# Optimization experiments

Hardware: AMD Instinct MI355X
Metric: run time of the kernel (lower is better)

## Reference

```python
import jax, jax.numpy as jnp
import numpy as np

D_MODEL = 512
N_HEADS = 8
HEAD_DIM = D_MODEL // N_HEADS
SEQ = 2048
BATCH = 2
EPS = 1e-5
SCALE = 1.0 / np.sqrt(HEAD_DIM).astype(np.float32)
# (kind, window, dilation) per head, matching init_kwargs head_specs
SPECS = [("global", 0, 1), ("global", 0, 1),
         ("window", 64, 1), ("window", 128, 1), ("window", 256, 1),
         ("dilated", 64, 2), ("dilated", 64, 4), ("dilated", 64, 8)]


def build_masks(N):
    i = jnp.arange(N)
    D = jnp.abs(i[:, None] - i[None, :])
    ms = []
    for kind, w, dil in SPECS:
        if kind == "global":
            ms.append(jnp.ones((N, N), dtype=bool))
        elif kind == "window":
            ms.append(D <= w)
        else:  # dilated
            ms.append((D % dil == 0) & (D // dil <= w))
    return jnp.stack(ms)  # [H, N, N] bool


def layernorm(x, g, b):
    mu = jnp.mean(x, axis=-1, keepdims=True)
    var = jnp.mean((x - mu) ** 2, axis=-1, keepdims=True)
    return (x - mu) * jax.lax.rsqrt(var + EPS) * g + b


def setup_inputs() -> dict:
    key = jax.random.key(0)
    ks = jax.random.split(key, 7)
    w = 0.02
    return {
        "x": jax.random.normal(ks[0], (BATCH, SEQ, D_MODEL), dtype=jnp.float32),
        "Wq": jax.random.normal(ks[1], (D_MODEL, D_MODEL), dtype=jnp.float32) * w,
        "Wk": jax.random.normal(ks[2], (D_MODEL, D_MODEL), dtype=jnp.float32) * w,
        "Wv": jax.random.normal(ks[3], (D_MODEL, D_MODEL), dtype=jnp.float32) * w,
        "Wo": jax.random.normal(ks[4], (D_MODEL, D_MODEL), dtype=jnp.float32) * w,
        "T_w1": jax.random.normal(ks[5], (D_MODEL, D_MODEL), dtype=jnp.float32) * w,
        "T_b1": jnp.zeros((D_MODEL,), dtype=jnp.float32),
        "T_w2": jax.random.normal(ks[6], (1, D_MODEL), dtype=jnp.float32) * w,
        "T_b2": jnp.zeros((1,), dtype=jnp.float32),
        "ln_in_g": jnp.ones((D_MODEL,), dtype=jnp.float32),
        "ln_in_b": jnp.zeros((D_MODEL,), dtype=jnp.float32),
        "ln_out_g": jnp.ones((D_MODEL,), dtype=jnp.float32),
        "ln_out_b": jnp.zeros((D_MODEL,), dtype=jnp.float32),
    }


def reference(x, Wq, Wk, Wv, Wo, T_w1, T_b1, T_w2, T_b2,
              ln_in_g, ln_in_b, ln_out_g, ln_out_b):
    B, N, H = x.shape
    x0 = x
    xn = layernorm(x, ln_in_g, ln_in_b)
    # torch Linear: y = x @ W.T ; reshape to [B, h, N, d]
    def heads(W):
        return (xn @ W.T).reshape(B, N, N_HEADS, HEAD_DIM).transpose(0, 2, 1, 3)
    Q, K, V = heads(Wq), heads(Wk), heads(Wv)
    attn = jnp.einsum("bhqd,bhkd->bhqk", Q, K) * SCALE
    mask = build_masks(N)  # [h, N, N]
    attn = jnp.where(mask[None], attn, -jnp.inf)
    attn = jax.nn.softmax(attn, axis=-1)  # every row has diagonal unmasked
    out = jnp.einsum("bhqk,bhkd->bhqd", attn, V)
    out = out.transpose(0, 2, 1, 3).reshape(B, N, N_HEADS * HEAD_DIM)
    out = out @ Wo.T
    # tanh-gated softmax over sequence dim
    T_logits = jnp.tanh(xn @ T_w1.T + T_b1) @ T_w2.T + T_b2  # [B, N, 1]
    T = jax.nn.softmax(T_logits, axis=1)
    out = out * T
    return layernorm(out + x0, ln_out_g, ln_out_b)
```

## Files before the change

### kernel.cpp

```cpp
#include <hip/hip_runtime.h>
#include <math.h>

#define N_SEQ 2048
#define DM    512
#define NTOK  4096
#define NH    8
#define HD    64
#define NSLOT 32

typedef __attribute__((ext_vector_type(8))) short short8;
typedef __attribute__((ext_vector_type(4))) short short4_t;
typedef __attribute__((ext_vector_type(4))) float f32x4;

__device__ inline short f2bf(float x) {
    union { float f; unsigned u; } v; v.f = x;
    unsigned r = v.u + 0x7fff + ((v.u >> 16) & 1);
    return (short)(r >> 16);
}
__device__ inline float bf2f(short s) {
    union { unsigned u; float f; } v; v.u = ((unsigned)(unsigned short)s) << 16;
    return v.f;
}
__device__ inline unsigned pkbf(float a, float b) {
    return ((unsigned)(unsigned short)f2bf(b) << 16) | (unsigned)(unsigned short)f2bf(a);
}
__device__ inline float ftanh(float x) {
    float e = __expf(2.f * x);
    return 1.f - 2.f / (e + 1.f);
}

__device__ inline f32x4 mfma16(short8 a, short8 b, f32x4 c) {
    return __builtin_amdgcn_mfma_f32_16x16x32_bf16(a, b, c, 0, 0, 0);
}

__device__ __forceinline__ void async_cp16(const short* g, short* l) {
    __builtin_amdgcn_global_load_lds(
        (const __attribute__((address_space(1))) void*)g,
        (__attribute__((address_space(3))) void*)l, 16, 0, 0);
}

#define QSCALE 0.1803398875f

__global__ __launch_bounds__(256) void k_lncvt(
    const float* __restrict__ x, const float* __restrict__ g,
    const float* __restrict__ b, short* __restrict__ y, float* __restrict__ lg,
    const float* __restrict__ Wq, const float* __restrict__ Wk,
    const float* __restrict__ Wv, const float* __restrict__ Tw1,
    const float* __restrict__ Wo,
    short* __restrict__ wcat, short* __restrict__ wo) {
    int blk = blockIdx.x, t = threadIdx.x;
    if (blk < 2048) {
        int sub = t >> 7, tt = t & 127;
        int tk = blk * 2 + sub;
        if (tt == 0) lg[tk] = 0.f;
        float4 xv = ((const float4*)(x + (size_t)tk * DM))[tt];
        float s = xv.x + xv.y + xv.z + xv.w;
        float q = xv.x*xv.x + xv.y*xv.y + xv.z*xv.z + xv.w*xv.w;
        for (int o = 32; o; o >>= 1) { s += __shfl_down(s, o); q += __shfl_down(q, o); }
        __shared__ float ls[4], lq[4];
        if ((t & 63) == 0) { ls[t >> 6] = s; lq[t >> 6] = q; }
        __syncthreads();
        s = ls[sub * 2] + ls[sub * 2 + 1];
        q = lq[sub * 2] + lq[sub * 2 + 1];
        float mu = s * (1.f / DM);
        float var = q * (1.f / DM) - mu * mu;
        float rs = rsqrtf(var + 1e-5f);
        float4 gv = ((const float4*)g)[tt], bv = ((const float4*)b)[tt];
        short4_t o;
        o[0] = f2bf((xv.x - mu) * rs * gv.x + bv.x);
        o[1] = f2bf((xv.y - mu) * rs * gv.y + bv.y);
        o[2] = f2bf((xv.z - mu) * rs * gv.z + bv.z);
        o[3] = f2bf((xv.w - mu) * rs * gv.w + bv.w);
        *(short4_t*)&y[(size_t)tk * DM + tt * 4] = o;
    } else {
        int id = (blk - 2048) * 256 + t;
        if (id < 262144) {
            int z = id >> 16; int off = id & 65535;
            const float* s = (z == 0) ? Wq : (z == 1) ? Wk : (z == 2) ? Wv : Tw1;
            float4 v = ((const float4*)s)[off];
            short4_t o = {f2bf(v.x), f2bf(v.y), f2bf(v.z), f2bf(v.w)};
            *(short4_t*)(wcat + (size_t)z * 262144 + (size_t)off * 4) = o;
        } else {
            int off = id - 262144;
            float4 v = ((const float4*)Wo)[off];
            short4_t o = {f2bf(v.x), f2bf(v.y), f2bf(v.z), f2bf(v.w)};
            *(short4_t*)(wo + (size_t)off * 4) = o;
        }
    }
}

__global__ __launch_bounds__(256) void k_gemmqkvt(
    const short* __restrict__ A, const short* __restrict__ W,
    const float* __restrict__ Tb1, const float* __restrict__ Tw2,
    short* __restrict__ qb, short* __restrict__ kb, short* __restrict__ vtb,
    float* __restrict__ lg) {
    __shared__ union {
        struct { short As[128 * 32]; short Bs[128 * 32]; } s;
        short Ct[128 * 132];
    } u;
    short* As = u.s.As;
    short* Bs = u.s.Bs;
    int t = threadIdx.x;
    int lane = t & 63, w = t >> 6;
    int wy = w >> 1, wx = w & 1;
    int ln = lane & 15, q4 = lane >> 4;
    int c0 = blockIdx.x * 128, m0 = blockIdx.y * 128;
    int sr = t >> 2, sc = (t & 3) << 3;
    f32x4 acc[4][4];
    f32x4 zero = {0.f, 0.f, 0.f, 0.f};
    #pragma unroll
    for (int i = 0; i < 4; i++)
        #pragma unroll
        for (int j = 0; j < 4; j++) acc[i][j] = zero;
    for (int k0 = 0; k0 < DM; k0 += 32) {
        __syncthreads();
        async_cp16(&A[(size_t)(m0 + sr) * DM + k0 + sc],      &As[sr * 32 + sc]);
        async_cp16(&A[(size_t)(m0 + 64 + sr) * DM + k0 + sc], &As[(64 + sr) * 32 + sc]);
        async_cp16(&W[(size_t)(c0 + sr) * DM + k0 + sc],      &Bs[sr * 32 + sc]);
        async_cp16(&W[(size_t)(c0 + 64 + sr) * DM + k0 + sc], &Bs[(64 + sr) * 32 + sc]);
        __syncthreads();
        short8 af[4], bfr[4];
        #pragma unroll
        for (int i = 0; i < 4; i++)
            af[i] = *(short8*)&As[(wy * 64 + i * 16 + ln) * 32 + q4 * 8];
        #pragma unroll
        for (int j = 0; j < 4; j++)
            bfr[j] = *(short8*)&Bs[(wx * 64 + j * 16 + ln) * 32 + q4 * 8];
        #pragma unroll
        for (int i = 0; i < 4; i++)
            #pragma unroll
            for (int j = 0; j < 4; j++)
                acc[i][j] = mfma16(af[i], bfr[j], acc[i][j]);
    }
    int z = c0 >> 9;
    if (z < 2) {
        short* dst = (z == 0) ? qb : kb;
        float sc2 = (z == 0) ? QSCALE : 1.0f;
        #pragma unroll
        for (int i = 0; i < 4; i++)
            #pragma unroll
            for (int j = 0; j < 4; j++)
                #pragma unroll
                for (int r = 0; r < 4; r++) {
                    int row = m0 + wy * 64 + i * 16 + q4 * 4 + r;
                    int col = c0 + wx * 64 + j * 16 + ln;
                    int nin = col & 511;
                    int h = nin >> 6, d = nin & 63;
                    int bi = row >> 11, n = row & (N_SEQ - 1);
                    dst[(((size_t)bi * NH + h) * N_SEQ + n) * HD + d] =
                        f2bf(acc[i][j][r] * sc2);
                }
    } else if (z == 2) {
        __syncthreads();
        #pragma unroll
        for (int i = 0; i < 4; i++)
            #pragma unroll
            for (int j = 0; j < 4; j++) {
                int lcol = wx * 64 + j * 16 + ln;
                int lrow = wy * 64 + i * 16 + q4 * 4;
                short4_t o = {f2bf(acc[i][j][0]), f2bf(acc[i][j][1]),
                              f2bf(acc[i][j][2]), f2bf(acc[i][j][3])};
                *(short4_t*)&u.Ct[lcol * 132 + lrow] = o;
            }
        __syncthreads();
        int bi = m0 >> 11, n0 = m0 & (N_SEQ - 1);
        #pragma unroll
        for (int it = 0; it < 8; it++) {
            int id = t + 256 * it;
            int lcol = id >> 4, ch = id & 15;
            int nin = (c0 & 511) + lcol;
            int h = nin >> 6, d = nin & 63;
            short8 v = *(short8*)&u.Ct[lcol * 132 + ch * 8];
            *(short8*)&vtb[(((size_t)bi * NH + h) * HD + d) * N_SEQ + n0 + ch * 8] = v;
        }
    } else {
        #pragma unroll
        for (int i = 0; i < 4; i++) {
            #pragma unroll
            for (int r = 0; r < 4; r++) {
                float s = 0.f;
                #pragma unroll
                for (int j = 0; j < 4; j++) {
                    int tc = (c0 & 511) + wx * 64 + j * 16 + ln;
                    s += ftanh(acc[i][j][r] + Tb1[tc]) * Tw2[tc];
                }
                s += __shfl_xor(s, 1);
                s += __shfl_xor(s, 2);
                s += __shfl_xor(s, 4);
                s += __shfl_xor(s, 8);
                if (ln == 0) {
                    int row = m0 + wy * 64 + i * 16 + q4 * 4 + r;
                    atomicAdd(&lg[row], s);
                }
            }
        }
    }
}

__global__ __launch_bounds__(256) void k_attn(const short* __restrict__ qb,
                                              const short* __restrict__ kb,
                                              const short* __restrict__ vtb,
                                              short* __restrict__ P_O,
                                              float* __restrict__ P_ml) {
    __shared__ short Ks[64 * 72];
    __shared__ short Vt[64 * 72];
    __shared__ short Pa[4][16 * 72];
    int t = threadIdx.x;
    int lane = t & 63, w = t >> 6;
    int ln = lane & 15, q4 = lane >> 4;
    int slot = blockIdx.x, qt = blockIdx.y, bi = blockIdx.z;
    int q0 = qt * 64;
    int h, c, CS;
    if (slot < 8)        { h = 0; c = slot;      CS = 4; }
    else if (slot < 16)  { h = 1; c = slot - 8;  CS = 4; }
    else if (slot == 16) { h = 2; c = 0;         CS = 3; }
    else if (slot < 19)  { h = 3; c = slot - 17; CS = 3; }
    else if (slot < 22)  { h = 4; c = slot - 19; CS = 3; }
    else if (slot < 24)  { h = 5; c = slot - 22; CS = 3; }
    else if (slot < 27)  { h = 6; c = slot - 24; CS = 3; }
    else                 { h = 7; c = slot - 27; CS = 4; }
    int kind = (h < 2) ? 0 : (h < 5) ? 1 : 2;
    int wnd = (h == 2 || h >= 5) ? 64 : (h == 3) ? 128 : (h == 4) ? 256 : 0;
    int dsh = (h == 5) ? 1 : (h == 6) ? 2 : (h == 7) ? 3 : 0;
    int dmask = (1 << dsh) - 1;
    int wmax = (kind == 0) ? 0 : (wnd << dsh);
    int tLoU, tHiU;
    if (kind == 0) { tLoU = 0; tHiU = 31; }
    else { tLoU = (q0 - wmax) >> 6; tHiU = (q0 + 63 + wmax) >> 6; }
    int ktLo = tLoU + c * CS;
    int ktHi = ktLo + CS - 1;
    if (ktHi > tHiU) ktHi = tHiU;
    if (ktHi > 31) ktHi = 31;
    if (ktLo < 0) ktLo = 0;
    int p4 = (bi * 32 + qt) * NSLOT + slot;
    float* ml = P_ml + (size_t)p4 * 64;
    if (ktLo > ktHi) {
        if (t < 64) ml[t] = 0.f;
        return;
    }
    const size_t base = ((size_t)bi * NH + h) * N_SEQ * HD;
    const short* Q = qb + base;
    const short* K = kb + base;
    const short* Vg = vtb + base;
    short8 qa[2];
    {
        const short* qrow = Q + (size_t)(q0 + w * 16 + ln) * HD + q4 * 8;
        qa[0] = *(const short8*)qrow;
        qa[1] = *(const short8*)(qrow + 32);
    }
    int qi = q0 + w * 16 + ln;
    float l_i = 0.f;
    f32x4 OT[4];
    f32x4 zero = {0.f, 0.f, 0.f, 0.f};
    #pragma unroll
    for (int d = 0; d < 4; d++) OT[d] = zero;
    short* Paw = Pa[w];
    for (int kt = ktLo; kt <= ktHi; kt++) {
        int k0 = kt << 6;
        __syncthreads();
        #pragma unroll
        for (int i2 = 0; i2 < 2; i2++) {
            int id = t + 256 * i2;
            int r = id >> 3, cc = id & 7;
            *(short8*)&Ks[r * 72 + cc * 8] =
                *(const short8*)&K[(size_t)(k0 + r) * HD + cc * 8];
            *(short8*)&Vt[r * 72 + cc * 8] =
                *(const short8*)&Vg[(size_t)r * N_SEQ + k0 + cc * 8];
        }
        __syncthreads();
        f32x4 ST[4];
        #pragma unroll
        for (int nt = 0; nt < 4; nt++) ST[nt] = zero;
        #pragma unroll
        for (int nt = 0; nt < 4; nt++) {
            #pragma unroll
            for (int ks = 0; ks < 2; ks++) {
                short8 af = *(short8*)&Ks[(nt * 16 + ln) * 72 + ks * 32 + q4 * 8];
                ST[nt] = mfma16(af, qa[ks], ST[nt]);
            }
        }
        if (kind != 0) {
            #pragma unroll
            for (int nt = 0; nt < 4; nt++)
                #pragma unroll
                for (int r = 0; r < 4; r++) {
                    int key = k0 + nt * 16 + q4 * 4 + r;
                    int dlt = qi - key; dlt = (dlt < 0) ? -dlt : dlt;
                    int valid;
                    if (kind == 1) valid = (dlt <= wnd);
                    else valid = ((dlt & dmask) == 0) && ((dlt >> dsh) <= wnd);
                    if (!valid) ST[nt][r] = -1e30f;
                }
        }
        float rs = 0.f;
        #pragma unroll
        for (int nt = 0; nt < 4; nt++) {
            float p0 = exp2f(ST[nt][0]);
            float p1 = exp2f(ST[nt][1]);
            float p2 = exp2f(ST[nt][2]);
            float p3 = exp2f(ST[nt][3]);
            rs += (p0 + p1) + (p2 + p3);
            *(unsigned*)&Paw[ln * 72 + nt * 16 + q4 * 4]     = pkbf(p0, p1);
            *(unsigned*)&Paw[ln * 72 + nt * 16 + q4 * 4 + 2] = pkbf(p2, p3);
        }
        rs += __shfl_xor(rs, 16);
        rs += __shfl_xor(rs, 32);
        l_i += rs;
        short8 pb0 = *(short8*)&Paw[ln * 72 + q4 * 8];
        short8 pb1 = *(short8*)&Paw[ln * 72 + 32 + q4 * 8];
        #pragma unroll
        for (int dt = 0; dt < 4; dt++) {
            short8 a0 = *(short8*)&Vt[(dt * 16 + ln) * 72 + q4 * 8];
            short8 a1 = *(short8*)&Vt[(dt * 16 + ln) * 72 + 32 + q4 * 8];
            OT[dt] = mfma16(a0, pb0, OT[dt]);
            OT[dt] = mfma16(a1, pb1, OT[dt]);
        }
    }
    if (q4 == 0) ml[w * 16 + ln] = l_i;
    #pragma unroll
    for (int dt = 0; dt < 4; dt++) {
        *(unsigned*)&Paw[ln * 72 + dt * 16 + q4 * 4]     = pkbf(OT[dt][0], OT[dt][1]);
        *(unsigned*)&Paw[ln * 72 + dt * 16 + q4 * 4 + 2] = pkbf(OT[dt][2], OT[dt][3]);
    }
    short8 o0 = *(short8*)&Paw[ln * 72 + q4 * 16];
    short8 o1 = *(short8*)&Paw[ln * 72 + q4 * 16 + 8];
    short* Op = P_O + (size_t)p4 * 4096;
    *(short8*)&Op[(w * 16 + ln) * 64 + q4 * 16] = o0;
    *(short8*)&Op[(w * 16 + ln) * 64 + q4 * 16 + 8] = o1;
}

__global__ __launch_bounds__(256) void k_combgate(const short* __restrict__ P_O,
                                                  const float* __restrict__ P_ml,
                                                  short* __restrict__ ob,
                                                  const float* __restrict__ lg,
                                                  float* __restrict__ gate) {
    int blk = blockIdx.x, t = threadIdx.x;
    if (blk < 512) {
        const int hbase[8] = {0, 8, 16, 17, 19, 22, 24, 27};
        const int hcnt[8]  = {8, 8, 1, 2, 3, 2, 3, 5};
        int h = blk & 7, qt = (blk >> 3) & 31, bi = blk >> 8;
        int row = t >> 2, c0 = (t & 3) * 16;
        int pb = (bi * 32 + qt) * NSLOT + hbase[h];
        int cnt = hcnt[h];
        float l = 0.f;
        float acc[16];
        #pragma unroll
        for (int j = 0; j < 16; j++) acc[j] = 0.f;
        for (int s = 0; s < cnt; s++) {
            float ls = P_ml[(size_t)(pb + s) * 64 + row];
            if (ls > 0.f) {
                l += ls;
                const short* Op = P_O + (size_t)(pb + s) * 4096 + row * 64 + c0;
                short8 v0 = *(const short8*)Op;
                short8 v1 = *(const short8*)(Op + 8);
                #pragma unroll
                for (int j = 0; j < 8; j++) acc[j]     += bf2f(v0[j]);
                #pragma unroll
                for (int j = 0; j < 8; j++) acc[8 + j] += bf2f(v1[j]);
            }
        }
        float inv = 1.f / l;
        int n = qt * 64 + row;
        short8 o0, o1;
        #pragma unroll
        for (int j = 0; j < 8; j++) o0[j] = f2bf(acc[j] * inv);
        #pragma unroll
        for (int j = 0; j < 8; j++) o1[j] = f2bf(acc[8 + j] * inv);
        short* dst = ob + ((size_t)bi * N_SEQ + n) * DM + h * 64 + c0;
        *(short8*)dst = o0;
        *(short8*)(dst + 8) = o1;
    } else {
        __shared__ float rg[8];
        int b = blk - 512;
        float v[8];
        {
            float4 a0 = *(const float4*)&lg[b * N_SEQ + t * 8];
            float4 a1 = *(const float4*)&lg[b * N_SEQ + t * 8 + 4];
            v[0] = a0.x; v[1] = a0.y; v[2] = a0.z; v[3] = a0.w;
            v[4] = a1.x; v[5] = a1.y; v[6] = a1.z; v[7] = a1.w;
        }
        float m = v[0];
        #pragma unroll
        for (int j = 1; j < 8; j++) m = fmaxf(m, v[j]);
        for (int o = 32; o; o >>= 1) m = fmaxf(m, __shfl_down(m, o));
        if ((t & 63) == 0) rg[t >> 6] = m;
        __syncthreads();
        m = fmaxf(fmaxf(rg[0], rg[1]), fmaxf(rg[2], rg[3]));
        float e[8], s = 0.f;
        #pragma unroll
        for (int j = 0; j < 8; j++) { e[j] = __expf(v[j] - m); s += e[j]; }
        for (int o = 32; o; o >>= 1) s += __shfl_down(s, o);
        if ((t & 63) == 0) rg[4 + (t >> 6)] = s;
        __syncthreads();
        s = (rg[4] + rg[5]) + (rg[6] + rg[7]);
        float inv = 1.f / s;
        float4 o0 = {e[0] * inv, e[1] * inv, e[2] * inv, e[3] * inv};
        float4 o1 = {e[4] * inv, e[5] * inv, e[6] * inv, e[7] * inv};
        *(float4*)&gate[b * N_SEQ + t * 8] = o0;
        *(float4*)&gate[b * N_SEQ + t * 8 + 4] = o1;
    }
}

__global__ __launch_bounds__(256) void k_gemmpf(
    const short* __restrict__ A,
    const short* __restrict__ W,
    const float* __restrict__ gate,
    const float* __restrict__ x0,
    const float* __restrict__ g,
    const float* __restrict__ b,
    float* __restrict__ out) {
    __shared__ short As[32 * 32];
    __shared__ short Bs[512 * 32];
    __shared__ float redS[32][4], redQ[32][4];
    int t = threadIdx.x;
    int lane = t & 63, w = t >> 6;
    int ln = lane & 15, q4 = lane >> 4;
    int m0 = blockIdx.x * 32;
    f32x4 acc[2][8];
    f32x4 zero = {0.f, 0.f, 0.f, 0.f};
    #pragma unroll
    for (int i = 0; i < 2; i++)
        #pragma unroll
        for (int j = 0; j < 8; j++) acc[i][j] = zero;
    for (int k0 = 0; k0 < DM; k0 += 32) {
        __syncthreads();
        if (t < 128) {
            int r = t >> 2, c = (t & 3) << 3;
            async_cp16(&A[(size_t)(m0 + r) * DM + k0 + c], &As[r * 32 + c]);
        }
        #pragma unroll
        for (int it = 0; it < 8; it++) {
            int id = t + 256 * it;
            int r = id >> 2, c = (id & 3) << 3;
            async_cp16(&W[(size_t)r * DM + k0 + c], &Bs[r * 32 + c]);
        }
        __syncthreads();
        short8 af[2];
        af[0] = *(short8*)&As[(ln) * 32 + q4 * 8];
        af[1] = *(short8*)&As[(16 + ln) * 32 + q4 * 8];
        #pragma unroll
        for (int j = 0; j < 8; j++) {
            short8 bfr = *(short8*)&Bs[(w * 128 + j * 16 + ln) * 32 + q4 * 8];
            acc[0][j] = mfma16(af[0], bfr, acc[0][j]);
            acc[1][j] = mfma16(af[1], bfr, acc[1][j]);
        }
    }
    float gts[2][4];
    #pragma unroll
    for (int i = 0; i < 2; i++)
        #pragma unroll
        for (int r = 0; r < 4; r++)
            gts[i][r] = gate[m0 + i * 16 + q4 * 4 + r];
    float sS[2][4] = {}, sQ[2][4] = {};
    #pragma unroll
    for (int i = 0; i < 2; i++)
        #pragma unroll
        for (int j = 0; j < 8; j++) {
            int col = w * 128 + j * 16 + ln;
            #pragma unroll
            for (int r = 0; r < 4; r++) {
                int row = m0 + i * 16 + q4 * 4 + r;
                float y = acc[i][j][r] * gts[i][r] + x0[(size_t)row * DM + col];
                acc[i][j][r] = y;
                sS[i][r] += y;
                sQ[i][r] += y * y;
            }
        }
    #pragma unroll
    for (int o = 1; o < 16; o <<= 1) {
        #pragma unroll
        for (int i = 0; i < 2; i++)
            #pragma unroll
            for (int r = 0; r < 4; r++) {
                sS[i][r] += __shfl_xor(sS[i][r], o);
                sQ[i][r] += __shfl_xor(sQ[i][r], o);
            }
    }
    if (ln == 0) {
        #pragma unroll
        for (int i = 0; i < 2; i++)
            #pragma unroll
            for (int r = 0; r < 4; r++) {
                redS[i * 16 + q4 * 4 + r][w] = sS[i][r];
                redQ[i * 16 + q4 * 4 + r][w] = sQ[i][r];
            }
    }
    __syncthreads();
    #pragma unroll
    for (int i = 0; i < 2; i++) {
        #pragma unroll
        for (int r = 0; r < 4; r++) {
            int lr = i * 16 + q4 * 4 + r;
            float S = (redS[lr][0] + redS[lr][1]) + (redS[lr][2] + redS[lr][3]);
            float Qq = (redQ[lr][0] + redQ[lr][1]) + (redQ[lr][2] + redQ[lr][3]);
            float mu = S * (1.f / DM);
            float var = Qq * (1.f / DM) - mu * mu;
            float rsq = rsqrtf(var + 1e-5f);
            int row = m0 + lr;
            #pragma unroll
            for (int j = 0; j < 8; j++) {
                int col = w * 128 + j * 16 + ln;
                out[(size_t)row * DM + col] =
                    (acc[i][j][r] - mu) * rsq * g[col] + b[col];
            }
        }
    }
}

extern "C" void kernel_launch(void* const* d_in, const int* in_sizes, int n_in,
                              void* d_out, int out_size, void* d_ws, size_t ws_size,
                              hipStream_t stream) {
    (void)in_sizes; (void)n_in; (void)out_size; (void)ws_size;
    const float* x    = (const float*)d_in[0];
    const float* Wq   = (const float*)d_in[1];
    const float* Wk   = (const float*)d_in[2];
    const float* Wv   = (const float*)d_in[3];
    const float* Wo   = (const float*)d_in[4];
    const float* Tw1  = (const float*)d_in[5];
    const float* Tb1  = (const float*)d_in[6];
    const float* Tw2  = (const float*)d_in[7];
    const float* ling = (const float*)d_in[9];
    const float* linb = (const float*)d_in[10];
    const float* logg = (const float*)d_in[11];
    const float* logb = (const float*)d_in[12];
    float* out = (float*)d_out;

    const size_t SZ = (size_t)NTOK * DM;
    const int NPART = 2 * 32 * NSLOT;
    char* p = (char*)d_ws;
    short* xn   = (short*)p; p += SZ * 2;
    short* wcat = (short*)p; p += (size_t)2048 * DM * 2;
    short* wo   = (short*)p; p += (size_t)DM * DM * 2;
    short* qb   = (short*)p; p += SZ * 2;
    short* kb   = (short*)p; p += SZ * 2;
    short* vtb  = (short*)p; p += SZ * 2;
    short* obuf = (short*)p; p += SZ * 2;
    float* lg   = (float*)p; p += (size_t)NTOK * 4;
    float* gate = (float*)p; p += (size_t)NTOK * 4;
    float* P_ml = (float*)p; p += (size_t)NPART * 64 * 4;
    short* P_O  = (short*)p; p += (size_t)NPART * 4096 * 2;

    k_lncvt<<<3328, 256, 0, stream>>>(x, ling, linb, xn, lg,
                                      Wq, Wk, Wv, Tw1, Wo, wcat, wo);
    k_gemmqkvt<<<dim3(16, 32), 256, 0, stream>>>(xn, wcat, Tb1, Tw2,
                                                 qb, kb, vtb, lg);
    k_attn<<<dim3(NSLOT, 32, 2), 256, 0, stream>>>(qb, kb, vtb, P_O, P_ml);
    k_combgate<<<514, 256, 0, stream>>>(P_O, P_ml, obuf, lg, gate);
    k_gemmpf<<<128, 256, 0, stream>>>(obuf, wo, gate, x, logg, logb, out);
}
```

Measured before the change: 167.3 us.

## Split output projection and gated layernorm into separate tiled GEMM and row kernels

Replaces the fused output-projection + gate + residual + layernorm kernel, which used only 128 blocks each loading all of Wo per k-step, with two kernels. One is a 128x64-tiled GEMM over a 8x32 grid writing fp32 projections to workspace (aliasing the partial-attention buffer). The other is a per-token row kernel doing the gate, residual and layernorm. This aims to raise parallelism and cut redundant weight traffic, at the cost of an extra launch and a full fp32 round-trip of the projection through memory.

```diff
diff --git a/kernel.cpp b/kernel.cpp
--- a/kernel.cpp
+++ b/kernel.cpp
@@ -401,110 +401,85 @@
     }
 }
 
-__global__ __launch_bounds__(256) void k_gemmpf(
-    const short* __restrict__ A,
-    const short* __restrict__ W,
-    const float* __restrict__ gate,
-    const float* __restrict__ x0,
-    const float* __restrict__ g,
-    const float* __restrict__ b,
-    float* __restrict__ out) {
-    __shared__ short As[32 * 32];
-    __shared__ short Bs[512 * 32];
-    __shared__ float redS[32][4], redQ[32][4];
+__global__ __launch_bounds__(256) void k_gemmp(
+    const short* __restrict__ A, const short* __restrict__ W,
+    float* __restrict__ proj) {
+    __shared__ short As[128 * 32];
+    __shared__ short Bs[64 * 32];
     int t = threadIdx.x;
     int lane = t & 63, w = t >> 6;
+    int wy = w >> 1, wx = w & 1;
     int ln = lane & 15, q4 = lane >> 4;
-    int m0 = blockIdx.x * 32;
-    f32x4 acc[2][8];
+    int c0 = blockIdx.x * 64, m0 = blockIdx.y * 128;
+    int sr = t >> 2, sc = (t & 3) << 3;
+    f32x4 acc[4][2];
     f32x4 zero = {0.f, 0.f, 0.f, 0.f};
     #pragma unroll
-    for (int i = 0; i < 2; i++)
-        #pragma unroll
-        for (int j = 0; j < 8; j++) acc[i][j] = zero;
+    for (int i = 0; i < 4; i++) { acc[i][0] = zero; acc[i][1] = zero; }
     for (int k0 = 0; k0 < DM; k0 += 32) {
         __syncthreads();
-        if (t < 128) {
-            int r = t >> 2, c = (t & 3) << 3;
-            async_cp16(&A[(size_t)(m0 + r) * DM + k0 + c], &As[r * 32 + c]);
-        }
-        #pragma unroll
-        for (int it = 0; it < 8; it++) {
-            int id = t + 256 * it;
-            int r = id >> 2, c = (id & 3) << 3;
-            async_cp16(&W[(size_t)r * DM + k0 + c], &Bs[r * 32 + c]);
-        }
-        __syncthreads();
-        short8 af[2];
-        af[0] = *(short8*)&As[(ln) * 32 + q4 * 8];
-        af[1] = *(short8*)&As[(16 + ln) * 32 + q4 * 8];
-        #pragma unroll
-        for (int j = 0; j < 8; j++) {
-            short8 bfr = *(short8*)&Bs[(w * 128 + j * 16 + ln) * 32 + q4 * 8];
-            acc[0][j] = mfma16(af[0], bfr, acc[0][j]);
-            acc[1][j] = mfma16(af[1], bfr, acc[1][j]);
-        }
-    }
-    float gts[2][4];
+        async_cp16(&A[(size_t)(m0 + sr) * DM + k0 + sc],      &As[sr * 32 + sc]);
+        async_cp16(&A[(size_t)(m0 + 64 + sr) * DM + k0 + sc], &As[(64 + sr) * 32 + sc]);
+        if (sr < 64)
+            async_cp16(&W[(size_t)(c0 + sr) * DM + k0 + sc], &Bs[sr * 32 + sc]);
+        __syncthreads();
+        short8 af[4], bfr[2];
+        #pragma unroll
+        for (int i = 0; i < 4; i++)
+            af[i] = *(short8*)&As[(wy * 64 + i * 16 + ln) * 32 + q4 * 8];
+        #pragma unroll
+        for (int j = 0; j < 2; j++)
+            bfr[j] = *(short8*)&Bs[(wx * 32 + j * 16 + ln) * 32 + q4 * 8];
+        #pragma unroll
+        for (int i = 0; i < 4; i++)
+            #pragma unroll
+            for (int j = 0; j < 2; j++)
+                acc[i][j] = mfma16(af[i], bfr[j], acc[i][j]);
+    }
     #pragma unroll
-    for (int i = 0; i < 2; i++)
-        #pragma unroll
-        for (int r = 0; r < 4; r++)
-            gts[i][r] = gate[m0 + i * 16 + q4 * 4 + r];
-    float sS[2][4] = {}, sQ[2][4] = {};
-    #pragma unroll
-    for (int i = 0; i < 2; i++)
-        #pragma unroll
-        for (int j = 0; j < 8; j++) {
-            int col = w * 128 + j * 16 + ln;
+    for (int i = 0; i < 4; i++)
+        #pragma unroll
+        for (int j = 0; j < 2; j++)
             #pragma unroll
             for (int r = 0; r < 4; r++) {
-                int row = m0 + i * 16 + q4 * 4 + r;
-                float y = acc[i][j][r] * gts[i][r] + x0[(size_t)row * DM + col];
-                acc[i][j][r] = y;
-                sS[i][r] += y;
-                sQ[i][r] += y * y;
+                int row = m0 + wy * 64 + i * 16 + q4 * 4 + r;
+                int col = c0 + wx * 32 + j * 16 + ln;
+                proj[(size_t)row * DM + col] = acc[i][j][r];
             }
-        }
-    #pragma unroll
-    for (int o = 1; o < 16; o <<= 1) {
-        #pragma unroll
-        for (int i = 0; i < 2; i++)
-            #pragma unroll
-            for (int r = 0; r < 4; r++) {
-                sS[i][r] += __shfl_xor(sS[i][r], o);
-                sQ[i][r] += __shfl_xor(sQ[i][r], o);
-            }
-    }
-    if (ln == 0) {
-        #pragma unroll
-        for (int i = 0; i < 2; i++)
-            #pragma unroll
-            for (int r = 0; r < 4; r++) {
-                redS[i * 16 + q4 * 4 + r][w] = sS[i][r];
-                redQ[i * 16 + q4 * 4 + r][w] = sQ[i][r];
-            }
-    }
+}
+
+__global__ __launch_bounds__(128) void k_final(const float* __restrict__ proj,
+                                               const float* __restrict__ gate,
+                                               const float* __restrict__ x0,
+                                               const float* __restrict__ g,
+                                               const float* __restrict__ b,
+                                               float* __restrict__ out) {
+    int tk = blockIdx.x, t = threadIdx.x;
+    float gt = gate[tk];
+    float4 pv = ((const float4*)(proj + (size_t)tk * DM))[t];
+    float4 xv = ((const float4*)(x0 + (size_t)tk * DM))[t];
+    float4 y;
+    y.x = pv.x * gt + xv.x;
+    y.y = pv.y * gt + xv.y;
+    y.z = pv.z * gt + xv.z;
+    y.w = pv.w * gt + xv.w;
+    float s = y.x + y.y + y.z + y.w;
+    float q = y.x*y.x + y.y*y.y + y.z*y.z + y.w*y.w;
+    for (int o = 32; o; o >>= 1) { s += __shfl_down(s, o); q += __shfl_down(q, o); }
+    __shared__ float ls[2], lq[2];
+    if ((t & 63) == 0) { ls[t >> 6] = s; lq[t >> 6] = q; }
     __syncthreads();
-    #pragma unroll
-    for (int i = 0; i < 2; i++) {
-        #pragma unroll
-        for (int r = 0; r < 4; r++) {
-            int lr = i * 16 + q4 * 4 + r;
-            float S = (redS[lr][0] + redS[lr][1]) + (redS[lr][2] + redS[lr][3]);
-            float Qq = (redQ[lr][0] + redQ[lr][1]) + (redQ[lr][2] + redQ[lr][3]);
-            float mu = S * (1.f / DM);
-            float var = Qq * (1.f / DM) - mu * mu;
-            float rsq = rsqrtf(var + 1e-5f);
-            int row = m0 + lr;
-            #pragma unroll
-            for (int j = 0; j < 8; j++) {
-                int col = w * 128 + j * 16 + ln;
-                out[(size_t)row * DM + col] =
-                    (acc[i][j][r] - mu) * rsq * g[col] + b[col];
-            }
-        }
-    }
+    s = ls[0] + ls[1]; q = lq[0] + lq[1];
+    float mu = s * (1.f / DM);
+    float var = q * (1.f / DM) - mu * mu;
+    float rs = rsqrtf(var + 1e-5f);
+    float4 gv = ((const float4*)g)[t], bv = ((const float4*)b)[t];
+    float4 o;
+    o.x = (y.x - mu) * rs * gv.x + bv.x;
+    o.y = (y.y - mu) * rs * gv.y + bv.y;
+    o.z = (y.z - mu) * rs * gv.z + bv.z;
+    o.w = (y.w - mu) * rs * gv.w + bv.w;
+    ((float4*)(out + (size_t)tk * DM))[t] = o;
 }
 
 extern "C" void kernel_launch(void* const* d_in, const int* in_sizes, int n_in,
@@ -538,6 +513,7 @@
     float* lg   = (float*)p; p += (size_t)NTOK * 4;
     float* gate = (float*)p; p += (size_t)NTOK * 4;
     float* P_ml = (float*)p; p += (size_t)NPART * 64 * 4;
+    float* proj = (float*)p;
     short* P_O  = (short*)p; p += (size_t)NPART * 4096 * 2;
 
     k_lncvt<<<3328, 256, 0, stream>>>(x, ling, linb, xn, lg,
@@ -546,5 +522,6 @@
                                                  qb, kb, vtb, lg);
     k_attn<<<dim3(NSLOT, 32, 2), 256, 0, stream>>>(qb, kb, vtb, P_O, P_ml);
     k_combgate<<<514, 256, 0, stream>>>(P_O, P_ml, obuf, lg, gate);
-    k_gemmpf<<<128, 256, 0, stream>>>(obuf, wo, gate, x, logg, logb, out);
-}
+    k_gemmp<<<dim3(8, 32), 256, 0, stream>>>(obuf, wo, proj);
+    k_final<<<NTOK, 128, 0, stream>>>(proj, gate, x, logg, logb, out);
+}
```

Measured after the change: 167.3 us. No clear change (-0.1%).
